# Kernel optimization log

Measured on AMD Instinct MI355X. Metric: run time of the kernel, lower is better.

The kernel has to match this reference:

```python
import jax, jax.numpy as jnp
import numpy as np

B, S, T = 64, 64, 64          # batch, encoder seq len, decoder context_length
V, D, H, L = 32000, 512, 1024, 256  # vocab, embed, hidden, latent


def _gru_cell(x, h, W_ih, W_hh, b_ih, b_hh):
    # PyTorch GRUCell math. x:[B,D_in], h:[B,H]
    gi = x @ W_ih.T + b_ih            # [B,3H]
    gh = h @ W_hh.T + b_hh            # [B,3H]
    i_r, i_z, i_n = jnp.split(gi, 3, axis=-1)
    h_r, h_z, h_n = jnp.split(gh, 3, axis=-1)
    r = jax.nn.sigmoid(i_r + h_r)
    z = jax.nn.sigmoid(i_z + h_z)
    n = jnp.tanh(i_n + r * h_n)
    return (1.0 - z) * n + z * h


def setup_inputs() -> dict:
    key = jax.random.key(0)
    ks = jax.random.split(key, 16)
    s = 0.02
    inp = {
        "x": jax.random.randint(ks[0], (B, S), 0, V),
        "eps": jax.random.normal(ks[1], (B, L), dtype=jnp.float32),
        "E": jax.random.normal(ks[2], (V, D), dtype=jnp.float32) * s,
        # encoder GRU
        "W_ih_enc": jax.random.normal(ks[3], (3 * H, D), dtype=jnp.float32) * s,
        "W_hh_enc": jax.random.normal(ks[4], (3 * H, H), dtype=jnp.float32) * s,
        "b_ih_enc": jnp.zeros((3 * H,), jnp.float32),
        "b_hh_enc": jnp.zeros((3 * H,), jnp.float32),
        # latent heads
        "W_mu": jax.random.normal(ks[5], (L, H), dtype=jnp.float32) * s,
        "b_mu": jnp.zeros((L,), jnp.float32),
        "W_lv": jax.random.normal(ks[6], (L, H), dtype=jnp.float32) * s,
        "b_lv": jnp.zeros((L,), jnp.float32),
        # decoder proj_h: latent -> hidden
        "W_proj": jax.random.normal(ks[7], (H, L), dtype=jnp.float32) * s,
        "b_proj": jnp.zeros((H,), jnp.float32),
        # decoder GRU cell
        "W_ih_dec": jax.random.normal(ks[8], (3 * H, D), dtype=jnp.float32) * s,
        "W_hh_dec": jax.random.normal(ks[9], (3 * H, H), dtype=jnp.float32) * s,
        "b_ih_dec": jnp.zeros((3 * H,), jnp.float32),
        "b_hh_dec": jnp.zeros((3 * H,), jnp.float32),
        # output projection hidden -> vocab
        "W_out": jax.random.normal(ks[10], (V, H), dtype=jnp.float32) * s,
        "b_out": jnp.zeros((V,), jnp.float32),
    }
    return inp


def reference(x, eps, E, W_ih_enc, W_hh_enc, b_ih_enc, b_hh_enc,
              W_mu, b_mu, W_lv, b_lv, W_proj, b_proj,
              W_ih_dec, W_hh_dec, b_ih_dec, b_hh_dec, W_out, b_out):
    # --- encode ---
    xe = E[x]                                  # [B,S,D]
    h0 = jnp.zeros((x.shape[0], H), xe.dtype)

    def enc_step(h, xt):
        h = _gru_cell(xt, h, W_ih_enc, W_hh_enc, b_ih_enc, b_hh_enc)
        return h, None

    h_last, _ = jax.lax.scan(enc_step, h0, jnp.swapaxes(xe, 0, 1))  # scan over S
    mu = h_last @ W_mu.T + b_mu                # [B,L]
    logvar = h_last @ W_lv.T + b_lv            # [B,L]

    # --- reparametrize ---
    z = mu + eps * jnp.exp(0.5 * logvar)       # [B,L]

    h_dec0 = z @ W_proj.T + b_proj             # [B,H]
    x0 = jnp.zeros((x.shape[0], D), xe.dtype)  # step 0 input is None -> zeros

    def dec_step(carry, _):
        h, xin = carry
        h = _gru_cell(xin, h, W_ih_dec, W_hh_dec, b_ih_dec, b_hh_dec)
        logits = h @ W_out.T + b_out           # [B,V]
        nxt = jnp.argmax(logits, axis=-1)      # [B]
        return (h, E[nxt]), logits

    _, logits_seq = jax.lax.scan(dec_step, (h_dec0, x0), None, length=T)
    outputs = jnp.swapaxes(logits_seq, 0, 1)   # [B,T,V]
    return outputs, mu, logvar
```

## Files before the change

### kernel.cpp

```cpp
#include <hip/hip_runtime.h>

#define B_ 64
#define S_ 64
#define T_ 64
#define V_ 32000
#define D_ 512
#define H_ 1024
#define L_ 256

typedef _Float16 f16;
typedef __attribute__((ext_vector_type(4))) _Float16 f16x4;
typedef __attribute__((ext_vector_type(8))) _Float16 f16x8;
typedef __attribute__((ext_vector_type(16))) float f32x16;

#define INV2048 (1.0f / 2048.0f)

__device__ __forceinline__ void write_frag(f16* __restrict__ Aohi, f16* __restrict__ Aolo,
                                           int b, int j, float hv) {
  const f16 hi = (f16)hv;
  const f16 lo = (f16)((hv - (float)hi) * 2048.0f);
  const long long fo =
      (((long long)(b >> 5) * 64 + (j >> 4)) * 64 + ((b & 31) + 32 * ((j >> 3) & 1))) * 8 + (j & 7);
  Aohi[fo] = hi;
  Aolo[fo] = lo;
}

template <int K>
__global__ __launch_bounds__(256) void k_pack_wf(
    const float* __restrict__ W, f16* __restrict__ Bhi, f16* __restrict__ Blo)
{
  const int n = blockIdx.x;
  const int k = threadIdx.x * 4;
  if (k >= K) return;
  float4 w = *reinterpret_cast<const float4*>(W + (long long)n * K + k);
  float wv[4] = {w.x, w.y, w.z, w.w};
  f16x4 hi, lo;
#pragma unroll
  for (int i = 0; i < 4; ++i) {
    const f16 h = (f16)wv[i];
    hi[i] = h;
    lo[i] = (f16)((wv[i] - (float)h) * 2048.0f);
  }
  const int nt = n >> 5;
  const int lane = (n & 31) + 32 * ((k >> 3) & 1);
  const int ks = k >> 4;
  const long long off = (((long long)nt * (K / 16) + ks) * 64 + lane) * 8 + (k & 7);
  *reinterpret_cast<f16x4*>(Bhi + off) = hi;
  *reinterpret_cast<f16x4*>(Blo + off) = lo;
}

__global__ __launch_bounds__(128) void k_pack_xe(
    const int* __restrict__ x, const float* __restrict__ E,
    f16* __restrict__ XAhi, f16* __restrict__ XAlo)
{
  const int m = blockIdx.x;
  const int s = m >> 6, b = m & 63;
  const int k = threadIdx.x * 4;
  const long long tok = x[b * S_ + s];
  float4 w = *reinterpret_cast<const float4*>(E + tok * D_ + k);
  float wv[4] = {w.x, w.y, w.z, w.w};
  f16x4 hi, lo;
#pragma unroll
  for (int i = 0; i < 4; ++i) {
    const f16 h = (f16)wv[i];
    hi[i] = h;
    lo[i] = (f16)((wv[i] - (float)h) * 2048.0f);
  }
  const int mt = m >> 5;
  const int lane = (m & 31) + 32 * ((k >> 3) & 1);
  const int ks = k >> 4;
  const long long off = (((long long)mt * 32 + ks) * 64 + lane) * 8 + (k & 7);
  *reinterpret_cast<f16x4*>(XAhi + off) = hi;
  *reinterpret_cast<f16x4*>(XAlo + off) = lo;
}

__global__ __launch_bounds__(256) void k_gates_mfma(
    const f16* __restrict__ XAhi, const f16* __restrict__ XAlo,
    const f16* __restrict__ Bhi, const f16* __restrict__ Blo,
    const float* __restrict__ b_ih, float* __restrict__ Gi)
{
  __shared__ float cand[4][64][33];
  const int tid = threadIdx.x;
  const int lane = tid & 63;
  const int wv = __builtin_amdgcn_readfirstlane(tid >> 6);
  const int s = blockIdx.x / 24;
  const int ng = blockIdx.x % 24;
  const int nt = ng * 4 + wv;

  f32x16 aM0, aM1, aLa0, aLa1, aLb0, aLb1;
#pragma unroll
  for (int i = 0; i < 16; ++i) {
    aM0[i] = 0.f; aM1[i] = 0.f; aLa0[i] = 0.f; aLa1[i] = 0.f; aLb0[i] = 0.f; aLb1[i] = 0.f;
  }

  const f16x8* pB_h = reinterpret_cast<const f16x8*>(Bhi) + ((long long)nt * 32) * 64 + lane;
  const f16x8* pB_l = reinterpret_cast<const f16x8*>(Blo) + ((long long)nt * 32) * 64 + lane;
  const f16x8* pA_h = reinterpret_cast<const f16x8*>(XAhi) + ((long long)s * 64) * 64 + lane;
  const f16x8* pA_l = reinterpret_cast<const f16x8*>(XAlo) + ((long long)s * 64) * 64 + lane;

#pragma unroll 4
  for (int ks = 0; ks < 32; ++ks) {
    const int o = ks * 64;
    f16x8 bh = pB_h[o];
    f16x8 bl = pB_l[o];
    f16x8 a0 = pA_h[o];
    f16x8 a1 = pA_h[o + 32 * 64];
    f16x8 l0 = pA_l[o];
    f16x8 l1 = pA_l[o + 32 * 64];
    aM0 = __builtin_amdgcn_mfma_f32_32x32x16_f16(a0, bh, aM0, 0, 0, 0);
    aM1 = __builtin_amdgcn_mfma_f32_32x32x16_f16(a1, bh, aM1, 0, 0, 0);
    aLa0 = __builtin_amdgcn_mfma_f32_32x32x16_f16(a0, bl, aLa0, 0, 0, 0);
    aLa1 = __builtin_amdgcn_mfma_f32_32x32x16_f16(a1, bl, aLa1, 0, 0, 0);
    aLb0 = __builtin_amdgcn_mfma_f32_32x32x16_f16(l0, bh, aLb0, 0, 0, 0);
    aLb1 = __builtin_amdgcn_mfma_f32_32x32x16_f16(l1, bh, aLb1, 0, 0, 0);
  }

  {
    const int l = lane & 31;
    const int rbase = 4 * (lane >> 5);
#pragma unroll
    for (int reg = 0; reg < 16; ++reg) {
      const int row = (reg & 3) + 8 * (reg >> 2) + rbase;
      cand[wv][row][l] = aM0[reg] + (aLa0[reg] + aLb0[reg]) * INV2048;
      cand[wv][row + 32][l] = aM1[reg] + (aLa1[reg] + aLb1[reg]) * INV2048;
    }
  }
  __syncthreads();
  const int bn0 = ng * 128;
#pragma unroll
  for (int i = 0; i < 8; ++i) {
    const int idx = i * 256 + tid;
    const int b4 = (idx & 15) * 4;
    const int nl = idx >> 4;
    const float bi = b_ih[bn0 + nl];
    float4 o;
    o.x = cand[nl >> 5][b4 + 0][nl & 31] + bi;
    o.y = cand[nl >> 5][b4 + 1][nl & 31] + bi;
    o.z = cand[nl >> 5][b4 + 2][nl & 31] + bi;
    o.w = cand[nl >> 5][b4 + 3][nl & 31] + bi;
    *reinterpret_cast<float4*>(&Gi[((long long)s * (3 * H_) + bn0 + nl) * 64 + b4]) = o;
  }
}

__global__ __launch_bounds__(256) void k_hh_mfma(
    const f16* __restrict__ Ahi, const f16* __restrict__ Alo,
    const f16* __restrict__ Bhi, const f16* __restrict__ Blo,
    float* __restrict__ preH)
{
  __shared__ float cand[4][64][33];
  const int tid = threadIdx.x;
  const int lane = tid & 63;
  const int wv = __builtin_amdgcn_readfirstlane(tid >> 6);
  const int nt = blockIdx.x;

  f32x16 aM0, aM1, aLa0, aLa1, aLb0, aLb1;
#pragma unroll
  for (int i = 0; i < 16; ++i) {
    aM0[i] = 0.f; aM1[i] = 0.f; aLa0[i] = 0.f; aLa1[i] = 0.f; aLb0[i] = 0.f; aLb1[i] = 0.f;
  }

  const f16x8* pB_h = reinterpret_cast<const f16x8*>(Bhi) + ((long long)nt * 64 + wv * 16) * 64 + lane;
  const f16x8* pB_l = reinterpret_cast<const f16x8*>(Blo) + ((long long)nt * 64 + wv * 16) * 64 + lane;
  const f16x8* pA_h = reinterpret_cast<const f16x8*>(Ahi) + (long long)(wv * 16) * 64 + lane;
  const f16x8* pA_l = reinterpret_cast<const f16x8*>(Alo) + (long long)(wv * 16) * 64 + lane;

#pragma unroll 4
  for (int q = 0; q < 16; ++q) {
    const int o = q * 64;
    f16x8 bh = pB_h[o];
    f16x8 bl = pB_l[o];
    f16x8 a0 = pA_h[o];
    f16x8 a1 = pA_h[o + 4096];
    f16x8 l0 = pA_l[o];
    f16x8 l1 = pA_l[o + 4096];
    aM0 = __builtin_amdgcn_mfma_f32_32x32x16_f16(a0, bh, aM0, 0, 0, 0);
    aM1 = __builtin_amdgcn_mfma_f32_32x32x16_f16(a1, bh, aM1, 0, 0, 0);
    aLa0 = __builtin_amdgcn_mfma_f32_32x32x16_f16(a0, bl, aLa0, 0, 0, 0);
    aLa1 = __builtin_amdgcn_mfma_f32_32x32x16_f16(a1, bl, aLa1, 0, 0, 0);
    aLb0 = __builtin_amdgcn_mfma_f32_32x32x16_f16(l0, bh, aLb0, 0, 0, 0);
    aLb1 = __builtin_amdgcn_mfma_f32_32x32x16_f16(l1, bh, aLb1, 0, 0, 0);
  }

  {
    const int l = lane & 31;
    const int rbase = 4 * (lane >> 5);
#pragma unroll
    for (int reg = 0; reg < 16; ++reg) {
      const int row = (reg & 3) + 8 * (reg >> 2) + rbase;
      cand[wv][row][l] = aM0[reg] + (aLa0[reg] + aLb0[reg]) * INV2048;
      cand[wv][row + 32][l] = aM1[reg] + (aLa1[reg] + aLb1[reg]) * INV2048;
    }
  }
  __syncthreads();
#pragma unroll
  for (int i = 0; i < 8; ++i) {
    const int idx = i * 256 + tid;
    const int b = idx & 63;
    const int l = idx >> 6;
    const float v = cand[0][b][l] + cand[1][b][l] + cand[2][b][l] + cand[3][b][l];
    preH[((long long)nt * 32 + l) * 64 + b] = v;
  }
}

__global__ __launch_bounds__(256) void k_apply_enc(
    const float* __restrict__ preH, const float* __restrict__ Gi_t,
    const float* __restrict__ b_hh,
    const float* __restrict__ hT_in, float* __restrict__ hT_out,
    f16* __restrict__ Aohi, f16* __restrict__ Aolo)
{
  const int idx = blockIdx.x * 256 + threadIdx.x;
  const int b = idx & 63;
  const int j = idx >> 6;
  const float gr = preH[(long long)j * 64 + b] + Gi_t[(long long)j * 64 + b] + b_hh[j];
  const float gz = preH[(long long)(H_ + j) * 64 + b] + Gi_t[(long long)(H_ + j) * 64 + b] + b_hh[H_ + j];
  const float gin = Gi_t[(long long)(2 * H_ + j) * 64 + b];
  const float ghn = preH[(long long)(2 * H_ + j) * 64 + b] + b_hh[2 * H_ + j];
  const float r = 1.f / (1.f + expf(-gr));
  const float z = 1.f / (1.f + expf(-gz));
  const float n = tanhf(fmaf(r, ghn, gin));
  const float hp = hT_in[(long long)j * 64 + b];
  const float hv = (1.f - z) * n + z * hp;
  hT_out[(long long)j * 64 + b] = hv;
  write_frag(Aohi, Aolo, b, j, hv);
}

template <int XMODE>
__global__ __launch_bounds__(1024) void k_dec_apply(
    const float* __restrict__ E, const unsigned long long* __restrict__ bp,
    const float* __restrict__ W_ih,
    const float* __restrict__ b_ih, const float* __restrict__ b_hh,
    const float* __restrict__ preH, const float* __restrict__ hT_in,
    float* __restrict__ hT_out, f16* __restrict__ Aohi, f16* __restrict__ Aolo)
{
  __shared__ float4 a_lds[64 * 64];
  __shared__ float red[12 * 3 * 64];
  __shared__ int toks[64];
  const int tid = threadIdx.x;
  const int lane = tid & 63;
  const int wv = __builtin_amdgcn_readfirstlane(tid >> 6);
  const int jj = wv & 3;
  const int ks = wv >> 2;
  const int j = blockIdx.x * 4 + jj;
  const int kf16 = tid & 63;
  const int msub = tid >> 6;

  float accR = 0.f, accZ = 0.f, accIN = 0.f;

  if constexpr (XMODE == 2) {
#pragma unroll
    for (int rr = 0; rr < 4; ++rr) {
      const int r = wv + rr * 16;
      unsigned long long kk = 0ull;
#pragma unroll
      for (int i = 0; i < 4; ++i) {
        const unsigned long long q = bp[(long long)r * 256 + lane + i * 64];
        if (q > kk) kk = q;
      }
#pragma unroll
      for (int m = 1; m < 64; m <<= 1) {
        const unsigned long long q = __shfl_xor(kk, m, 64);
        if (q > kk) kk = q;
      }
      if (lane == 0) toks[r] = (int)(0xFFFFFFFFu - (unsigned)(kk & 0xFFFFFFFFull));
    }
    __syncthreads();

    const float* wr = W_ih + (long long)j * D_;
    const float* wz = W_ih + (long long)(j + H_) * D_;
    const float* wn = W_ih + (long long)(j + 2 * H_) * D_;
    for (int c = 0; c < 2; ++c) {
      __syncthreads();
#pragma unroll
      for (int p = 0; p < 4; ++p) {
        const int m = p * 16 + msub;
        const long long tok = toks[m];
        float4 v = *reinterpret_cast<const float4*>(E + tok * D_ + c * 256 + kf16 * 4);
        a_lds[m * 64 + (kf16 ^ (m & 7))] = v;
      }
      __syncthreads();
#pragma unroll 4
      for (int q = 0; q < 16; ++q) {
        const int kf = ks * 16 + q;
        float4 a = a_lds[lane * 64 + (kf ^ (lane & 7))];
        float4 w0 = *reinterpret_cast<const float4*>(wr + c * 256 + kf * 4);
        float4 w1 = *reinterpret_cast<const float4*>(wz + c * 256 + kf * 4);
        float4 w2 = *reinterpret_cast<const float4*>(wn + c * 256 + kf * 4);
        accR = fmaf(w0.x, a.x, accR); accR = fmaf(w0.y, a.y, accR);
        accR = fmaf(w0.z, a.z, accR); accR = fmaf(w0.w, a.w, accR);
        accZ = fmaf(w1.x, a.x, accZ); accZ = fmaf(w1.y, a.y, accZ);
        accZ = fmaf(w1.z, a.z, accZ); accZ = fmaf(w1.w, a.w, accZ);
        accIN = fmaf(w2.x, a.x, accIN); accIN = fmaf(w2.y, a.y, accIN);
        accIN = fmaf(w2.z, a.z, accIN); accIN = fmaf(w2.w, a.w, accIN);
      }
    }
  }

  if (ks > 0) {
    float* rp = red + (((ks - 1) * 4 + jj) * 3) * 64 + lane;
    rp[0] = accR; rp[64] = accZ; rp[128] = accIN;
  }
  __syncthreads();
  if (ks == 0) {
#pragma unroll
    for (int t2 = 0; t2 < 3; ++t2) {
      const float* rp = red + ((t2 * 4 + jj) * 3) * 64 + lane;
      accR += rp[0]; accZ += rp[64]; accIN += rp[128];
    }
    const float gr = accR + preH[(long long)j * 64 + lane] + b_ih[j] + b_hh[j];
    const float gz = accZ + preH[(long long)(H_ + j) * 64 + lane] + b_ih[H_ + j] + b_hh[H_ + j];
    const float gin = accIN + b_ih[2 * H_ + j];
    const float ghn = preH[(long long)(2 * H_ + j) * 64 + lane] + b_hh[2 * H_ + j];
    const float r = 1.f / (1.f + expf(-gr));
    const float z = 1.f / (1.f + expf(-gz));
    const float n = tanhf(fmaf(r, ghn, gin));
    const float hp = hT_in[(long long)j * 64 + lane];
    const float hv = (1.f - z) * n + z * hp;
    hT_out[(long long)j * 64 + lane] = hv;
    write_frag(Aohi, Aolo, lane, j, hv);
  }
}

__global__ __launch_bounds__(256) void k_logits_hh(
    const f16* __restrict__ Ahi, const f16* __restrict__ Alo,
    const f16* __restrict__ WOhi, const f16* __restrict__ WOlo,
    const f16* __restrict__ WHhi, const f16* __restrict__ WHlo,
    const float* __restrict__ b_out, float* __restrict__ out,
    unsigned long long* __restrict__ bestPart, float* __restrict__ preH, int t)
{
  __shared__ float cand[4][64][33];
  __shared__ unsigned long long wbest[4][64];
  const int tid = threadIdx.x;
  const int lane = tid & 63;
  const int wv = __builtin_amdgcn_readfirstlane(tid >> 6);

  if (blockIdx.x >= 250) {
    const int hhb = blockIdx.x - 250;
    const int nt = hhb * 4 + wv;
    f32x16 aM0, aM1, aLa0, aLa1, aLb0, aLb1;
#pragma unroll
    for (int i = 0; i < 16; ++i) {
      aM0[i] = 0.f; aM1[i] = 0.f; aLa0[i] = 0.f; aLa1[i] = 0.f; aLb0[i] = 0.f; aLb1[i] = 0.f;
    }
    const f16x8* pB_h = reinterpret_cast<const f16x8*>(WHhi) + ((long long)nt * 64) * 64 + lane;
    const f16x8* pB_l = reinterpret_cast<const f16x8*>(WHlo) + ((long long)nt * 64) * 64 + lane;
    const f16x8* pA_h = reinterpret_cast<const f16x8*>(Ahi) + lane;
    const f16x8* pA_l = reinterpret_cast<const f16x8*>(Alo) + lane;
#pragma unroll 4
    for (int ksi = 0; ksi < 64; ++ksi) {
      const int o = ksi * 64;
      f16x8 bh = pB_h[o];
      f16x8 bl = pB_l[o];
      f16x8 a0 = pA_h[o];
      f16x8 a1 = pA_h[o + 4096];
      f16x8 l0 = pA_l[o];
      f16x8 l1 = pA_l[o + 4096];
      aM0 = __builtin_amdgcn_mfma_f32_32x32x16_f16(a0, bh, aM0, 0, 0, 0);
      aM1 = __builtin_amdgcn_mfma_f32_32x32x16_f16(a1, bh, aM1, 0, 0, 0);
      aLa0 = __builtin_amdgcn_mfma_f32_32x32x16_f16(a0, bl, aLa0, 0, 0, 0);
      aLa1 = __builtin_amdgcn_mfma_f32_32x32x16_f16(a1, bl, aLa1, 0, 0, 0);
      aLb0 = __builtin_amdgcn_mfma_f32_32x32x16_f16(l0, bh, aLb0, 0, 0, 0);
      aLb1 = __builtin_amdgcn_mfma_f32_32x32x16_f16(l1, bh, aLb1, 0, 0, 0);
    }
    {
      const int l = lane & 31;
      const int rbase = 4 * (lane >> 5);
#pragma unroll
      for (int reg = 0; reg < 16; ++reg) {
        const int row = (reg & 3) + 8 * (reg >> 2) + rbase;
        cand[wv][row][l] = aM0[reg] + (aLa0[reg] + aLb0[reg]) * INV2048;
        cand[wv][row + 32][l] = aM1[reg] + (aLa1[reg] + aLb1[reg]) * INV2048;
      }
    }
    __syncthreads();
#pragma unroll
    for (int i = 0; i < 8; ++i) {
      const int idx = i * 256 + tid;
      const int b4 = (idx & 15) * 4;
      const int nl = idx >> 4;
      float4 o;
      o.x = cand[nl >> 5][b4 + 0][nl & 31];
      o.y = cand[nl >> 5][b4 + 1][nl & 31];
      o.z = cand[nl >> 5][b4 + 2][nl & 31];
      o.w = cand[nl >> 5][b4 + 3][nl & 31];
      *reinterpret_cast<float4*>(&preH[((long long)hhb * 128 + nl) * 64 + b4]) = o;
    }
    return;
  }

  const int nt = blockIdx.x * 4 + wv;
  f32x16 accM0, accM1, accL0, accL1;
#pragma unroll
  for (int i = 0; i < 16; ++i) { accM0[i] = 0.f; accM1[i] = 0.f; accL0[i] = 0.f; accL1[i] = 0.f; }

  const f16x8* pAh0 = reinterpret_cast<const f16x8*>(Ahi) + lane;
  const f16x8* pAh1 = reinterpret_cast<const f16x8*>(Ahi) + 4096 + lane;
  const f16x8* pAl0 = reinterpret_cast<const f16x8*>(Alo) + lane;
  const f16x8* pAl1 = reinterpret_cast<const f16x8*>(Alo) + 4096 + lane;
  const f16x8* pBh = reinterpret_cast<const f16x8*>(WOhi) + (long long)nt * 4096 + lane;
  const f16x8* pBl = reinterpret_cast<const f16x8*>(WOlo) + (long long)nt * 4096 + lane;

#pragma unroll 4
  for (int ksi = 0; ksi < 64; ++ksi) {
    const int o = ksi * 64;
    f16x8 bh = pBh[o];
    f16x8 bl = pBl[o];
    f16x8 ah0 = pAh0[o];
    f16x8 ah1 = pAh1[o];
    f16x8 al0 = pAl0[o];
    f16x8 al1 = pAl1[o];
    accM0 = __builtin_amdgcn_mfma_f32_32x32x16_f16(ah0, bh, accM0, 0, 0, 0);
    accM1 = __builtin_amdgcn_mfma_f32_32x32x16_f16(ah1, bh, accM1, 0, 0, 0);
    accL0 = __builtin_amdgcn_mfma_f32_32x32x16_f16(ah0, bl, accL0, 0, 0, 0);
    accL1 = __builtin_amdgcn_mfma_f32_32x32x16_f16(ah1, bl, accL1, 0, 0, 0);
    accL0 = __builtin_amdgcn_mfma_f32_32x32x16_f16(al0, bh, accL0, 0, 0, 0);
    accL1 = __builtin_amdgcn_mfma_f32_32x32x16_f16(al1, bh, accL1, 0, 0, 0);
  }

  const int nn = nt * 32 + (lane & 31);
  const float bo = b_out[nn];
  const int rbase = 4 * (lane >> 5);
#pragma unroll
  for (int reg = 0; reg < 16; ++reg) {
    const int row0 = (reg & 3) + 8 * (reg >> 2) + rbase;
    const float v0 = accM0[reg] + accL0[reg] * INV2048 + bo;
    __builtin_nontemporal_store(v0, &out[(long long)row0 * (T_ * (long long)V_) + (long long)t * V_ + nn]);
    cand[wv][row0][lane & 31] = v0;
    const int row1 = row0 + 32;
    const float v1 = accM1[reg] + accL1[reg] * INV2048 + bo;
    __builtin_nontemporal_store(v1, &out[(long long)row1 * (T_ * (long long)V_) + (long long)t * V_ + nn]);
    cand[wv][row1][lane & 31] = v1;
  }
  __syncthreads();
  {
    const int w = tid >> 6, r = tid & 63;
    const int nb = (blockIdx.x * 4 + w) * 32;
    unsigned long long kk = 0ull;
#pragma unroll
    for (int l0 = 0; l0 < 32; ++l0) {
      const int l = (l0 + r) & 31;
      const float v = cand[w][r][l];
      unsigned u = __float_as_uint(v);
      u = (u & 0x80000000u) ? ~u : (u | 0x80000000u);
      const unsigned long long key = ((unsigned long long)u << 32) |
          (unsigned long long)(0xFFFFFFFFu - (unsigned)(nb + l));
      if (key > kk) kk = key;
    }
    wbest[w][r] = kk;
  }
  __syncthreads();
  if (tid < 64) {
    unsigned long long kk = wbest[0][tid];
#pragma unroll
    for (int w = 1; w < 4; ++w) { const unsigned long long q = wbest[w][tid]; if (q > kk) kk = q; }
    bestPart[(long long)tid * 256 + blockIdx.x] = kk;
  }
}

__global__ __launch_bounds__(256) void k_mu_lv_z(
    const float* __restrict__ hT, const float* __restrict__ W_mu, const float* __restrict__ b_mu,
    const float* __restrict__ W_lv, const float* __restrict__ b_lv,
    const float* __restrict__ eps, float* __restrict__ out_mu, float* __restrict__ out_lv,
    float* __restrict__ zT)
{
  const int lane = threadIdx.x & 63;
  const int wv = __builtin_amdgcn_readfirstlane(threadIdx.x >> 6);
  const int l = blockIdx.x * 4 + wv;
  const float* wm = W_mu + (long long)l * H_;
  const float* wl = W_lv + (long long)l * H_;
  float am = 0.f, av = 0.f;
#pragma unroll 8
  for (int k = 0; k < H_; ++k) {
    const float h = hT[k * 64 + lane];
    am = fmaf(wm[k], h, am);
    av = fmaf(wl[k], h, av);
  }
  const float mu = am + b_mu[l];
  const float lv = av + b_lv[l];
  out_mu[lane * L_ + l] = mu;
  out_lv[lane * L_ + l] = lv;
  zT[l * 64 + lane] = fmaf(eps[lane * L_ + l], expf(0.5f * lv), mu);
}

__global__ __launch_bounds__(256) void k_proj(
    const float* __restrict__ zT, const float* __restrict__ W_proj,
    const float* __restrict__ b_proj, float* __restrict__ hT0,
    f16* __restrict__ Aohi, f16* __restrict__ Aolo)
{
  const int lane = threadIdx.x & 63;
  const int wv = __builtin_amdgcn_readfirstlane(threadIdx.x >> 6);
  const int j = blockIdx.x * 4 + wv;
  const float* wr = W_proj + (long long)j * L_;
  float acc = 0.f;
#pragma unroll 8
  for (int k = 0; k < L_; ++k) acc = fmaf(wr[k], zT[k * 64 + lane], acc);
  const float hv = acc + b_proj[j];
  hT0[(long long)j * 64 + lane] = hv;
  write_frag(Aohi, Aolo, lane, j, hv);
}

extern "C" void kernel_launch(void* const* d_in, const int* in_sizes, int n_in,
                              void* d_out, int out_size, void* d_ws, size_t ws_size,
                              hipStream_t stream) {
  (void)in_sizes; (void)n_in; (void)out_size;
  const int*   x        = (const int*)d_in[0];
  const float* eps      = (const float*)d_in[1];
  const float* E        = (const float*)d_in[2];
  const float* W_ih_enc = (const float*)d_in[3];
  const float* W_hh_enc = (const float*)d_in[4];
  const float* b_ih_enc = (const float*)d_in[5];
  const float* b_hh_enc = (const float*)d_in[6];
  const float* W_mu     = (const float*)d_in[7];
  const float* b_mu     = (const float*)d_in[8];
  const float* W_lv     = (const float*)d_in[9];
  const float* b_lv     = (const float*)d_in[10];
  const float* W_proj   = (const float*)d_in[11];
  const float* b_proj   = (const float*)d_in[12];
  const float* W_ih_dec = (const float*)d_in[13];
  const float* W_hh_dec = (const float*)d_in[14];
  const float* b_ih_dec = (const float*)d_in[15];
  const float* b_hh_dec = (const float*)d_in[16];
  const float* W_out    = (const float*)d_in[17];
  const float* b_out    = (const float*)d_in[18];

  float* out = (float*)d_out;
  const long long OFF_MU = (long long)B_ * T_ * V_;
  const long long OFF_LV = OFF_MU + (long long)B_ * L_;

  float* ws = (float*)d_ws;
  float* hA   = ws + 0;
  float* hB   = ws + 65536;
  float* dA   = ws + 131072;
  float* dB   = ws + 196608;
  float* zT   = ws + 262144;
  unsigned long long* bestPart = (unsigned long long*)(ws + 278528);
  float* preH = ws + 311296;
  f16* frAhi  = (f16*)(ws + 507904);
  f16* frAlo  = (f16*)(ws + 540672);
  f16* WHEhi  = (f16*)(ws + 638976);
  f16* WHElo  = (f16*)(ws + 2211840);
  f16* WHDhi  = (f16*)(ws + 3784704);
  f16* WHDlo  = (f16*)(ws + 5357568);
  f16* WIEhi  = (f16*)(ws + 6930432);
  f16* WIElo  = (f16*)(ws + 7716864);
  f16* XAhi   = (f16*)(ws + 8503296);
  f16* XAlo   = (f16*)(ws + 9551872);
  float* Gi   = ws + 10600448;
  f16* WOhi   = (f16*)(ws + 8503296);
  f16* WOlo   = (f16*)(ws + 24887296);
  const size_t WS_NEED = (size_t)41271296 * 4;
  if (ws_size < WS_NEED) return;

  hipMemsetAsync(hA, 0, (size_t)H_ * B_ * sizeof(float), stream);
  hipMemsetAsync(frAhi, 0, (size_t)2 * 65536 * sizeof(f16), stream);
  hipMemsetAsync(bestPart, 0, (size_t)64 * 256 * 8, stream);

  k_pack_wf<1024><<<3 * H_, 256, 0, stream>>>(W_hh_enc, WHEhi, WHElo);
  k_pack_wf<1024><<<3 * H_, 256, 0, stream>>>(W_hh_dec, WHDhi, WHDlo);
  k_pack_wf<512><<<3 * H_, 128, 0, stream>>>(W_ih_enc, WIEhi, WIElo);
  k_pack_xe<<<S_ * B_, 128, 0, stream>>>(x, E, XAhi, XAlo);

  k_gates_mfma<<<64 * 24, 256, 0, stream>>>(XAhi, XAlo, WIEhi, WIElo, b_ih_enc, Gi);

  for (int t = 0; t < S_; ++t) {
    const float* hin = (t & 1) ? hB : hA;
    float* hout = (t & 1) ? hA : hB;
    k_hh_mfma<<<96, 256, 0, stream>>>(frAhi, frAlo, WHEhi, WHElo, preH);
    k_apply_enc<<<256, 256, 0, stream>>>(preH, Gi + (long long)t * 3 * H_ * B_,
                                         b_hh_enc, hin, hout, frAhi, frAlo);
  }

  k_mu_lv_z<<<64, 256, 0, stream>>>(hA, W_mu, b_mu, W_lv, b_lv, eps,
                                    out + OFF_MU, out + OFF_LV, zT);
  k_proj<<<256, 256, 0, stream>>>(zT, W_proj, b_proj, dA, frAhi, frAlo);

  k_pack_wf<1024><<<V_, 256, 0, stream>>>(W_out, WOhi, WOlo);

  k_hh_mfma<<<96, 256, 0, stream>>>(frAhi, frAlo, WHDhi, WHDlo, preH);

  for (int t = 0; t < T_; ++t) {
    const float* hin = (t & 1) ? dB : dA;
    float* hout = (t & 1) ? dA : dB;
    if (t == 0) {
      k_dec_apply<0><<<256, 1024, 0, stream>>>(
          E, nullptr, W_ih_dec, b_ih_dec, b_hh_dec, preH, hin, hout, frAhi, frAlo);
    } else {
      k_dec_apply<2><<<256, 1024, 0, stream>>>(
          E, bestPart, W_ih_dec, b_ih_dec, b_hh_dec, preH, hin, hout, frAhi, frAlo);
    }
    k_logits_hh<<<274, 256, 0, stream>>>(frAhi, frAlo, WOhi, WOlo, WHDhi, WHDlo,
                                         b_out, out, bestPart, preH, t);
  }
}
```

Baseline: 6.076 ms.

## Split logits K dimension across wave pairs and double logits grid

The logits kernel now assigns two waves per 32-column vocab tile, each covering half of the hidden dimension. Partial sums are combined through shared memory before the bias add, the store and the per-block argmax. The grid grows from 250 to 500 logits blocks and bestPart is widened to 512 partials per row, with the decoder apply kernel updated to reduce over 8 chunks. The aim is more parallelism and better latency hiding on the bandwidth-bound W_out stream, at the cost of an extra sync and shared-memory reduction. Hidden-state ping-pong buffers are also collapsed to in-place updates, which relies on each thread reading its own h element before writing it.

Measured after the change: 6.257 ms. 1.03x slower.

```diff
diff --git a/kernel.cpp b/kernel.cpp
--- a/kernel.cpp
+++ b/kernel.cpp
@@ -252,8 +252,8 @@
       const int r = wv + rr * 16;
       unsigned long long kk = 0ull;
 #pragma unroll
-      for (int i = 0; i < 4; ++i) {
-        const unsigned long long q = bp[(long long)r * 256 + lane + i * 64];
+      for (int i = 0; i < 8; ++i) {
+        const unsigned long long q = bp[(long long)r * 512 + lane + i * 64];
         if (q > kk) kk = q;
       }
 #pragma unroll
@@ -333,8 +333,8 @@
   const int lane = tid & 63;
   const int wv = __builtin_amdgcn_readfirstlane(tid >> 6);
 
-  if (blockIdx.x >= 250) {
-    const int hhb = blockIdx.x - 250;
+  if (blockIdx.x >= 500) {
+    const int hhb = blockIdx.x - 500;
     const int nt = hhb * 4 + wv;
     f32x16 aM0, aM1, aLa0, aLa1, aLb0, aLb1;
 #pragma unroll
@@ -387,20 +387,24 @@
     return;
   }
 
-  const int nt = blockIdx.x * 4 + wv;
+  const int p = wv >> 1;
+  const int kh = wv & 1;
+  const int nt = blockIdx.x * 2 + p;
+
   f32x16 accM0, accM1, accL0, accL1;
 #pragma unroll
   for (int i = 0; i < 16; ++i) { accM0[i] = 0.f; accM1[i] = 0.f; accL0[i] = 0.f; accL1[i] = 0.f; }
 
-  const f16x8* pAh0 = reinterpret_cast<const f16x8*>(Ahi) + lane;
-  const f16x8* pAh1 = reinterpret_cast<const f16x8*>(Ahi) + 4096 + lane;
-  const f16x8* pAl0 = reinterpret_cast<const f16x8*>(Alo) + lane;
-  const f16x8* pAl1 = reinterpret_cast<const f16x8*>(Alo) + 4096 + lane;
-  const f16x8* pBh = reinterpret_cast<const f16x8*>(WOhi) + (long long)nt * 4096 + lane;
-  const f16x8* pBl = reinterpret_cast<const f16x8*>(WOlo) + (long long)nt * 4096 + lane;
+  const int kb = kh * 32 * 64;
+  const f16x8* pAh0 = reinterpret_cast<const f16x8*>(Ahi) + kb + lane;
+  const f16x8* pAh1 = reinterpret_cast<const f16x8*>(Ahi) + 4096 + kb + lane;
+  const f16x8* pAl0 = reinterpret_cast<const f16x8*>(Alo) + kb + lane;
+  const f16x8* pAl1 = reinterpret_cast<const f16x8*>(Alo) + 4096 + kb + lane;
+  const f16x8* pBh = reinterpret_cast<const f16x8*>(WOhi) + (long long)nt * 4096 + kb + lane;
+  const f16x8* pBl = reinterpret_cast<const f16x8*>(WOlo) + (long long)nt * 4096 + kb + lane;
 
 #pragma unroll 4
-  for (int ksi = 0; ksi < 64; ++ksi) {
+  for (int ksi = 0; ksi < 32; ++ksi) {
     const int o = ksi * 64;
     f16x8 bh = pBh[o];
     f16x8 bl = pBl[o];
@@ -416,29 +420,44 @@
     accL1 = __builtin_amdgcn_mfma_f32_32x32x16_f16(al1, bh, accL1, 0, 0, 0);
   }
 
-  const int nn = nt * 32 + (lane & 31);
-  const float bo = b_out[nn];
+  const int l31 = lane & 31;
   const int rbase = 4 * (lane >> 5);
-#pragma unroll
-  for (int reg = 0; reg < 16; ++reg) {
-    const int row0 = (reg & 3) + 8 * (reg >> 2) + rbase;
-    const float v0 = accM0[reg] + accL0[reg] * INV2048 + bo;
-    __builtin_nontemporal_store(v0, &out[(long long)row0 * (T_ * (long long)V_) + (long long)t * V_ + nn]);
-    cand[wv][row0][lane & 31] = v0;
-    const int row1 = row0 + 32;
-    const float v1 = accM1[reg] + accL1[reg] * INV2048 + bo;
-    __builtin_nontemporal_store(v1, &out[(long long)row1 * (T_ * (long long)V_) + (long long)t * V_ + nn]);
-    cand[wv][row1][lane & 31] = v1;
+
+  if (kh == 1) {
+#pragma unroll
+    for (int reg = 0; reg < 16; ++reg) {
+      const int row0 = (reg & 3) + 8 * (reg >> 2) + rbase;
+      cand[2 + p][row0][l31] = accM0[reg] + accL0[reg] * INV2048;
+      cand[2 + p][row0 + 32][l31] = accM1[reg] + accL1[reg] * INV2048;
+    }
+  }
+  __syncthreads();
+  if (kh == 0) {
+    const int nn = nt * 32 + l31;
+    const float bo = b_out[nn];
+#pragma unroll
+    for (int reg = 0; reg < 16; ++reg) {
+      const int row0 = (reg & 3) + 8 * (reg >> 2) + rbase;
+      const float v0 = accM0[reg] + accL0[reg] * INV2048 + cand[2 + p][row0][l31] + bo;
+      __builtin_nontemporal_store(v0, &out[(long long)row0 * (T_ * (long long)V_) + (long long)t * V_ + nn]);
+      const int row1 = row0 + 32;
+      const float v1 = accM1[reg] + accL1[reg] * INV2048 + cand[2 + p][row1][l31] + bo;
+      __builtin_nontemporal_store(v1, &out[(long long)row1 * (T_ * (long long)V_) + (long long)t * V_ + nn]);
+      cand[2 + p][row0][l31] = v0;
+      cand[2 + p][row1][l31] = v1;
+    }
   }
   __syncthreads();
   {
-    const int w = tid >> 6, r = tid & 63;
-    const int nb = (blockIdx.x * 4 + w) * 32;
+    const int w = tid >> 6;
+    const int s = w & 1;
+    const int r = tid & 63;
+    const int nb = (blockIdx.x * 2 + s) * 32;
     unsigned long long kk = 0ull;
 #pragma unroll
     for (int l0 = 0; l0 < 32; ++l0) {
       const int l = (l0 + r) & 31;
-      const float v = cand[w][r][l];
+      const float v = cand[2 + s][r][l];
       unsigned u = __float_as_uint(v);
       u = (u & 0x80000000u) ? ~u : (u | 0x80000000u);
       const unsigned long long key = ((unsigned long long)u << 32) |
@@ -452,7 +471,7 @@
     unsigned long long kk = wbest[0][tid];
 #pragma unroll
     for (int w = 1; w < 4; ++w) { const unsigned long long q = wbest[w][tid]; if (q > kk) kk = q; }
-    bestPart[(long long)tid * 256 + blockIdx.x] = kk;
+    bestPart[(long long)tid * 512 + blockIdx.x] = kk;
   }
 }
 
@@ -528,31 +547,29 @@
 
   float* ws = (float*)d_ws;
   float* hA   = ws + 0;
-  float* hB   = ws + 65536;
-  float* dA   = ws + 131072;
-  float* dB   = ws + 196608;
-  float* zT   = ws + 262144;
-  unsigned long long* bestPart = (unsigned long long*)(ws + 278528);
-  float* preH = ws + 311296;
-  f16* frAhi  = (f16*)(ws + 507904);
-  f16* frAlo  = (f16*)(ws + 540672);
-  f16* WHEhi  = (f16*)(ws + 638976);
-  f16* WHElo  = (f16*)(ws + 2211840);
-  f16* WHDhi  = (f16*)(ws + 3784704);
-  f16* WHDlo  = (f16*)(ws + 5357568);
-  f16* WIEhi  = (f16*)(ws + 6930432);
-  f16* WIElo  = (f16*)(ws + 7716864);
-  f16* XAhi   = (f16*)(ws + 8503296);
-  f16* XAlo   = (f16*)(ws + 9551872);
-  float* Gi   = ws + 10600448;
-  f16* WOhi   = (f16*)(ws + 8503296);
-  f16* WOlo   = (f16*)(ws + 24887296);
-  const size_t WS_NEED = (size_t)41271296 * 4;
+  float* dA   = ws + 65536;
+  float* zT   = ws + 131072;
+  unsigned long long* bestPart = (unsigned long long*)(ws + 147456);
+  float* preH = ws + 212992;
+  f16* frAhi  = (f16*)(ws + 409600);
+  f16* frAlo  = (f16*)(ws + 442368);
+  f16* WHEhi  = (f16*)(ws + 475136);
+  f16* WHElo  = (f16*)(ws + 2048000);
+  f16* WHDhi  = (f16*)(ws + 3620864);
+  f16* WHDlo  = (f16*)(ws + 5193728);
+  f16* WIEhi  = (f16*)(ws + 6766592);
+  f16* WIElo  = (f16*)(ws + 7553024);
+  f16* XAhi   = (f16*)(ws + 8339456);
+  f16* XAlo   = (f16*)(ws + 9388032);
+  float* Gi   = ws + 10436608;
+  f16* WOhi   = (f16*)(ws + 8339456);
+  f16* WOlo   = (f16*)(ws + 24723456);
+  const size_t WS_NEED = (size_t)41107456 * 4;
   if (ws_size < WS_NEED) return;
 
   hipMemsetAsync(hA, 0, (size_t)H_ * B_ * sizeof(float), stream);
   hipMemsetAsync(frAhi, 0, (size_t)2 * 65536 * sizeof(f16), stream);
-  hipMemsetAsync(bestPart, 0, (size_t)64 * 256 * 8, stream);
+  hipMemsetAsync(bestPart, 0, (size_t)64 * 512 * 8, stream);
 
   k_pack_wf<1024><<<3 * H_, 256, 0, stream>>>(W_hh_enc, WHEhi, WHElo);
   k_pack_wf<1024><<<3 * H_, 256, 0, stream>>>(W_hh_dec, WHDhi, WHDlo);
@@ -562,11 +579,9 @@
   k_gates_mfma<<<64 * 24, 256, 0, stream>>>(XAhi, XAlo, WIEhi, WIElo, b_ih_enc, Gi);
 
   for (int t = 0; t < S_; ++t) {
-    const float* hin = (t & 1) ? hB : hA;
-    float* hout = (t & 1) ? hA : hB;
     k_hh_mfma<<<96, 256, 0, stream>>>(frAhi, frAlo, WHEhi, WHElo, preH);
     k_apply_enc<<<256, 256, 0, stream>>>(preH, Gi + (long long)t * 3 * H_ * B_,
-                                         b_hh_enc, hin, hout, frAhi, frAlo);
+                                         b_hh_enc, hA, hA, frAhi, frAlo);
   }
 
   k_mu_lv_z<<<64, 256, 0, stream>>>(hA, W_mu, b_mu, W_lv, b_lv, eps,
@@ -578,16 +593,14 @@
   k_hh_mfma<<<96, 256, 0, stream>>>(frAhi, frAlo, WHDhi, WHDlo, preH);
 
   for (int t = 0; t < T_; ++t) {
-    const float* hin = (t & 1) ? dB : dA;
-    float* hout = (t & 1) ? dA : dB;
     if (t == 0) {
       k_dec_apply<0><<<256, 1024, 0, stream>>>(
-          E, nullptr, W_ih_dec, b_ih_dec, b_hh_dec, preH, hin, hout, frAhi, frAlo);
+          E, nullptr, W_ih_dec, b_ih_dec, b_hh_dec, preH, dA, dA, frAhi, frAlo);
     } else {
       k_dec_apply<2><<<256, 1024, 0, stream>>>(
-          E, bestPart, W_ih_dec, b_ih_dec, b_hh_dec, preH, hin, hout, frAhi, frAlo);
-    }
-    k_logits_hh<<<274, 256, 0, stream>>>(frAhi, frAlo, WOhi, WOlo, WHDhi, WHDlo,
+          E, bestPart, W_ih_dec, b_ih_dec, b_hh_dec, preH, dA, dA, frAhi, frAlo);
+    }
+    k_logits_hh<<<524, 256, 0, stream>>>(frAhi, frAlo, WOhi, WOlo, WHDhi, WHDlo,
                                          b_out, out, bestPart, preH, t);
   }
 }
```
